# Kernel optimization log

Hardware: AMD Instinct MI355X
Metric: run time of the kernel (lower is better)

The kernel has to match this reference:

```python
import jax, jax.numpy as jnp
import numpy as np

N_OBJ, P, M, D = 8, 65536, 32, 128


def setup_inputs() -> dict:
    key = jax.random.key(0)
    k1, k2, k3 = jax.random.split(key, 3)
    net_out = jax.random.normal(k1, (N_OBJ * P, D), dtype=jnp.float32)
    # cumulative end offsets per object; last entry (unused by the loop) repeats N_total
    pt_offset = jnp.concatenate([
        jnp.arange(1, N_OBJ + 1, dtype=jnp.int32) * P,
        jnp.array([N_OBJ * P], dtype=jnp.int32),
    ])
    mask_pts = jax.random.randint(k2, (N_OBJ, M, P), 0, 2, dtype=jnp.int32)
    mask_embs = jax.random.normal(k3, (N_OBJ * M, D), dtype=jnp.float32)
    logit_scale = jnp.ones((1,), dtype=jnp.float32)
    return {
        "net_out": net_out,
        "pt_offset": pt_offset,
        "mask_embs": mask_embs,
        "mask_pts": mask_pts,
        "logit_scale": logit_scale,
    }


def reference(net_out, pt_offset, mask_embs, mask_pts, logit_scale):
    # Uniform segments: object o owns points [o*P, (o+1)*P), matching pt_offset.
    n_obj, n_masks, n_pts = mask_pts.shape
    d = net_out.shape[1]
    x = net_out[: n_obj * n_pts].reshape(n_obj, n_pts, d)          # [O,P,D]
    emb = jnp.nan_to_num(
        mask_embs.reshape(n_obj, n_masks, d), nan=0.0, posinf=0.0, neginf=0.0
    )                                                               # [O,M,D]
    m = mask_pts.astype(net_out.dtype)                              # [O,M,P]

    # sum_p mask * ||x_p - e||^2 = sum_p m*||x_p||^2 + cnt*||e||^2 - 2 e . (sum_p m x_p)
    cnt = jnp.sum(m, axis=-1)                                       # [O,M]
    xsq = jnp.sum(x * x, axis=-1)                                   # [O,P]
    t1 = jnp.einsum("omp,op->om", m, xsq)                          # [O,M]
    t2 = cnt * jnp.sum(emb * emb, axis=-1)                          # [O,M]
    mx = jnp.einsum("omp,opd->omd", m, x)                          # [O,M,D]
    t3 = 2.0 * jnp.sum(emb * mx, axis=-1)                           # [O,M]

    sum_sq = jnp.sum(t1 + t2 - t3)
    total_points = jnp.sum(cnt)
    # torch: sum over masks of MSE(masked_pts, label)*n_pts, divided by total points
    # MSE*n_pts = sum_sq_per_mask / D; empty masks contribute 0 to both terms.
    return jnp.where(total_points > 0, sum_sq / (d * total_points), 0.0)
```

## Files before the change

kernel.cpp:

```cpp
#include <hip/hip_runtime.h>
#include <math.h>

#define NOBJ 8
#define NP   65536
#define NM   32
#define ND   128
#define CHUNKS 64
#define PTS_WG 1024
#define PTS_WAVE 128

__launch_bounds__(512, 4)
__global__ void distill_main(const float* __restrict__ net,
                             const float* __restrict__ embs,
                             const int* __restrict__ mask,
                             float* __restrict__ ws) {
  __shared__ float T[8 * 16 * ND];
  __shared__ float esq[NM];
  __shared__ int   Wlds[PTS_WG];
  __shared__ float red[8][4];

  const int tid  = threadIdx.x;
  const int wave = tid >> 6;
  const int lane = tid & 63;
  const int o     = blockIdx.x >> 6;
  const int chunk = blockIdx.x & (CHUNKS - 1);

  const float* EB = embs + (size_t)o * NM * ND;

  if (tid < NM) {
    float a = 0.f;
    const float* e = EB + (size_t)tid * ND;
    for (int d_ = 0; d_ < ND; ++d_) {
      float v = e[d_];
      if (!isfinite(v)) v = 0.f;
      a += v * v;
    }
    esq[tid] = a;
  }

  for (int j = 0; j < 32; ++j) {
    int idx = j * 512 + tid;
    int d_ = idx & (ND - 1);
    int n  = (idx >> 7) & 15;
    int g  = idx >> 11;
    float acc = 0.f;
#pragma unroll
    for (int b = 0; b < 4; ++b) {
      float e = EB[(size_t)(g * 4 + b) * ND + d_];
      if (!isfinite(e)) e = 0.f;
      acc += ((n >> b) & 1) ? e : 0.f;
    }
    T[idx] = acc;
  }
  __syncthreads();

  const int p0 = chunk * PTS_WG + wave * PTS_WAVE;
  const int* mp = mask + (size_t)o * NM * NP + p0 + 2 * lane;
  int W0 = 0, W1 = 0;
  float pB = 0.f, TPl = 0.f;
  int2 v[8], u[8];
#pragma unroll
  for (int j = 0; j < 8; ++j) v[j] = *(const int2*)(mp + (size_t)j * NP);
#pragma unroll
  for (int b = 0; b < 4; ++b) {
    if (b < 3) {
#pragma unroll
      for (int j = 0; j < 8; ++j)
        u[j] = *(const int2*)(mp + (size_t)((b + 1) * 8 + j) * NP);
    }
#pragma unroll
    for (int j = 0; j < 8; ++j) {
      const int m = b * 8 + j;
      int b0 = (v[j].x != 0), b1 = (v[j].y != 0);
      W0 |= b0 << m; W1 |= b1 << m;
      float c = (float)(b0 + b1);
      TPl += c;
      pB  += esq[m] * c;
    }
    if (b < 3) {
#pragma unroll
      for (int j = 0; j < 8; ++j) v[j] = u[j];
    }
  }
  *(int2*)&Wlds[wave * PTS_WAVE + 2 * lane] = make_int2(W0, W1);
  __syncthreads();

  const float* xo = net + ((size_t)o * NP + p0) * ND;
  const int half = lane >> 5;
  const int dl   = (lane & 31) * 4;
  const int base = wave * PTS_WAVE;
  float accA = 0.f, accC = 0.f;

  auto comp = [&](const float4 X, const int W) {
    accA += (float)__popc(W) * (X.x * X.x + X.y * X.y + X.z * X.z + X.w * X.w);
    float s0 = 0.f, s1 = 0.f, s2 = 0.f, s3 = 0.f;
#pragma unroll
    for (int g = 0; g < 8; ++g) {
      int n = (W >> (g * 4)) & 15;
      const float4 t = *(const float4*)&T[(g * 16 + n) * ND + dl];
      s0 += t.x; s1 += t.y; s2 += t.z; s3 += t.w;
    }
    accC += s0 * X.x + s1 * X.y + s2 * X.z + s3 * X.w;
  };

  float4 Xa0 = *(const float4*)(xo + (size_t)(0 + half) * ND + dl);
  float4 Xa1 = *(const float4*)(xo + (size_t)(2 + half) * ND + dl);
  float4 Xb0 = *(const float4*)(xo + (size_t)(4 + half) * ND + dl);
  float4 Xb1 = *(const float4*)(xo + (size_t)(6 + half) * ND + dl);
  int Wq0 = Wlds[base + 0 + half], Wq1 = Wlds[base + 2 + half];
  int Wq2 = Wlds[base + 4 + half], Wq3 = Wlds[base + 6 + half];

  for (int i = 0; i < PTS_WAVE; i += 8) {
    int pf = i + 8;
    pf = (pf < PTS_WAVE) ? pf : 0;
    float4 Ta0 = *(const float4*)(xo + (size_t)(pf + 0 + half) * ND + dl);
    float4 Ta1 = *(const float4*)(xo + (size_t)(pf + 2 + half) * ND + dl);
    float4 Tb0 = *(const float4*)(xo + (size_t)(pf + 4 + half) * ND + dl);
    float4 Tb1 = *(const float4*)(xo + (size_t)(pf + 6 + half) * ND + dl);
    int Tw0 = Wlds[base + pf + 0 + half], Tw1 = Wlds[base + pf + 2 + half];
    int Tw2 = Wlds[base + pf + 4 + half], Tw3 = Wlds[base + pf + 6 + half];

    comp(Xa0, Wq0);
    comp(Xa1, Wq1);
    comp(Xb0, Wq2);
    comp(Xb1, Wq3);

    Xa0 = Ta0; Xa1 = Ta1; Xb0 = Tb0; Xb1 = Tb1;
    Wq0 = Tw0; Wq1 = Tw1; Wq2 = Tw2; Wq3 = Tw3;
  }

#pragma unroll
  for (int off = 32; off >= 1; off >>= 1) {
    accA += __shfl_xor(accA, off, 64);
    accC += __shfl_xor(accC, off, 64);
    pB   += __shfl_xor(pB,   off, 64);
    TPl  += __shfl_xor(TPl,  off, 64);
  }
  if (lane == 0) {
    red[wave][0] = accA; red[wave][1] = pB;
    red[wave][2] = accC; red[wave][3] = TPl;
  }
  __syncthreads();
  if (tid == 0) {
    float A = 0.f, B = 0.f, C = 0.f, TP = 0.f;
    for (int w = 0; w < 8; ++w) {
      A += red[w][0]; B += red[w][1]; C += red[w][2]; TP += red[w][3];
    }
    atomicAdd(&ws[0], A);
    atomicAdd(&ws[1], B);
    atomicAdd(&ws[2], C);
    atomicAdd(&ws[3], TP);
  }
}

__global__ void distill_final(const float* __restrict__ ws, float* __restrict__ out) {
  float A = ws[0], B = ws[1], C = ws[2], TP = ws[3];
  out[0] = (TP > 0.f) ? (A + B - 2.f * C) / ((float)ND * TP) : 0.f;
}

extern "C" void kernel_launch(void* const* d_in, const int* in_sizes, int n_in,
                              void* d_out, int out_size, void* d_ws, size_t ws_size,
                              hipStream_t stream) {
  const float* net  = (const float*)d_in[0];
  const float* embs = (const float*)d_in[2];
  const int*   mask = (const int*)d_in[3];
  float* ws = (float*)d_ws;

  hipMemsetAsync(d_ws, 0, 4 * sizeof(float), stream);
  distill_main<<<NOBJ * CHUNKS, 512, 0, stream>>>(net, embs, mask, ws);
  distill_final<<<1, 1, 0, stream>>>(ws, (float*)d_out);
}
```

Baseline: 423.8 us.

## Overlap mask/net loads with LUT build and drop barrier before main loop

Issues the first mask loads before the lookup-table setup and hoists the first net_out prefetch ahead of the mask packing, so global memory latency overlaps the prologue work. The 16-entry subset-sum table is now built from four loaded embedding values per thread using pairwise partial sums, which cuts redundant global loads. The workgroup barrier after writing the per-wave mask words is replaced by an LDS wait, since each wave reads only its own Wlds region. This relies on that wave-local access pattern for correctness and adds register pressure from the extra live prefetches.

```diff
diff --git a/kernel.cpp b/kernel.cpp
--- a/kernel.cpp
+++ b/kernel.cpp
@@ -27,40 +27,55 @@
 
   const float* EB = embs + (size_t)o * NM * ND;
 
+  const int p0 = chunk * PTS_WG + wave * PTS_WAVE;
+  const int* mp = mask + (size_t)o * NM * NP + p0 + 2 * lane;
+  int2 v[8], u[8];
+#pragma unroll
+  for (int j = 0; j < 8; ++j) v[j] = *(const int2*)(mp + (size_t)j * NP);
+
   if (tid < NM) {
     float a = 0.f;
     const float* e = EB + (size_t)tid * ND;
     for (int d_ = 0; d_ < ND; ++d_) {
-      float v = e[d_];
-      if (!isfinite(v)) v = 0.f;
-      a += v * v;
+      float x = e[d_];
+      if (!isfinite(x)) x = 0.f;
+      a += x * x;
     }
     esq[tid] = a;
   }
 
-  for (int j = 0; j < 32; ++j) {
-    int idx = j * 512 + tid;
-    int d_ = idx & (ND - 1);
-    int n  = (idx >> 7) & 15;
-    int g  = idx >> 11;
-    float acc = 0.f;
 #pragma unroll
-    for (int b = 0; b < 4; ++b) {
-      float e = EB[(size_t)(g * 4 + b) * ND + d_];
-      if (!isfinite(e)) e = 0.f;
-      acc += ((n >> b) & 1) ? e : 0.f;
-    }
-    T[idx] = acc;
+  for (int k = 0; k < 2; ++k) {
+    const int q  = tid + k * 512;
+    const int d_ = q & (ND - 1);
+    const int g  = q >> 7;
+    float e0 = EB[(size_t)(g * 4 + 0) * ND + d_];
+    float e1 = EB[(size_t)(g * 4 + 1) * ND + d_];
+    float e2 = EB[(size_t)(g * 4 + 2) * ND + d_];
+    float e3 = EB[(size_t)(g * 4 + 3) * ND + d_];
+    if (!isfinite(e0)) e0 = 0.f;
+    if (!isfinite(e1)) e1 = 0.f;
+    if (!isfinite(e2)) e2 = 0.f;
+    if (!isfinite(e3)) e3 = 0.f;
+    const float a01[4] = {0.f, e0, e1, e0 + e1};
+    const float a23[4] = {0.f, e2, e3, e2 + e3};
+    float* Tg = &T[(size_t)(g * 16) * ND + d_];
+#pragma unroll
+    for (int n = 0; n < 16; ++n)
+      Tg[(size_t)n * ND] = a01[n & 3] + a23[n >> 2];
   }
   __syncthreads();
 
-  const int p0 = chunk * PTS_WG + wave * PTS_WAVE;
-  const int* mp = mask + (size_t)o * NM * NP + p0 + 2 * lane;
+  const float* xo = net + ((size_t)o * NP + p0) * ND;
+  const int half = lane >> 5;
+  const int dl   = (lane & 31) * 4;
+  float4 Xa0 = *(const float4*)(xo + (size_t)(0 + half) * ND + dl);
+  float4 Xa1 = *(const float4*)(xo + (size_t)(2 + half) * ND + dl);
+  float4 Xb0 = *(const float4*)(xo + (size_t)(4 + half) * ND + dl);
+  float4 Xb1 = *(const float4*)(xo + (size_t)(6 + half) * ND + dl);
+
   int W0 = 0, W1 = 0;
   float pB = 0.f, TPl = 0.f;
-  int2 v[8], u[8];
-#pragma unroll
-  for (int j = 0; j < 8; ++j) v[j] = *(const int2*)(mp + (size_t)j * NP);
 #pragma unroll
   for (int b = 0; b < 4; ++b) {
     if (b < 3) {
@@ -83,11 +98,8 @@
     }
   }
   *(int2*)&Wlds[wave * PTS_WAVE + 2 * lane] = make_int2(W0, W1);
-  __syncthreads();
+  asm volatile("s_waitcnt lgkmcnt(0)" ::: "memory");
 
-  const float* xo = net + ((size_t)o * NP + p0) * ND;
-  const int half = lane >> 5;
-  const int dl   = (lane & 31) * 4;
   const int base = wave * PTS_WAVE;
   float accA = 0.f, accC = 0.f;
 
@@ -103,10 +115,6 @@
     accC += s0 * X.x + s1 * X.y + s2 * X.z + s3 * X.w;
   };
 
-  float4 Xa0 = *(const float4*)(xo + (size_t)(0 + half) * ND + dl);
-  float4 Xa1 = *(const float4*)(xo + (size_t)(2 + half) * ND + dl);
-  float4 Xb0 = *(const float4*)(xo + (size_t)(4 + half) * ND + dl);
-  float4 Xb1 = *(const float4*)(xo + (size_t)(6 + half) * ND + dl);
   int Wq0 = Wlds[base + 0 + half], Wq1 = Wlds[base + 2 + half];
   int Wq2 = Wlds[base + 4 + half], Wq3 = Wlds[base + 6 + half];
 
```

After: 427.5 us. About the same (+0.9%).
